# Performance work log

Hardware: AMD Instinct MI355X
Metric: run time of the kernel (lower is better)

## Reference

```python
import jax, jax.numpy as jnp
import numpy as np
from jax import lax

DN = ('NHWC', 'HWIO', 'NHWC')

def _prelu(x, a):
    return jnp.where(x >= 0, x, a * x)

def _conv(x, w, b):
    return lax.conv_general_dilated(x, w, (1, 1), 'VALID', dimension_numbers=DN) + b

def _maxpool(x, k, s, padding):
    # padding: list of (lo, hi) for all 4 dims, or 'VALID'
    return lax.reduce_window(x, -jnp.inf, lax.max, (1, k, k, 1), (1, s, s, 1), padding)

def _onet_forward(x, conv1_w, conv1_b, alpha1, conv2_w, conv2_b, alpha2,
                  conv3_w, conv3_b, alpha3, conv4_w, conv4_b, alpha4,
                  dense5_w, dense5_b, alpha5, w_cls, b_cls, w_box, b_box, w_pts, b_pts):
    # x: [B, 48, 48, 3]
    x = _prelu(_conv(x, conv1_w, conv1_b), alpha1)              # [B,46,46,32]
    # TF 'same' pooling: out=ceil(46/2)=23, total pad 1 -> pad (0,1) bottom/right
    x = _maxpool(x, 3, 2, [(0, 0), (0, 1), (0, 1), (0, 0)])     # [B,23,23,32]
    x = _prelu(_conv(x, conv2_w, conv2_b), alpha2)              # [B,21,21,64]
    x = _maxpool(x, 3, 2, 'VALID')                              # [B,10,10,64]
    x = _prelu(_conv(x, conv3_w, conv3_b), alpha3)              # [B,8,8,64]
    x = _maxpool(x, 2, 2, 'VALID')                              # [B,4,4,64]
    x = _prelu(_conv(x, conv4_w, conv4_b), alpha4)              # [B,3,3,128]
    # Permute((3,2,1)): (H,W,C) -> (C,W,H), then row-major flatten -> 1152
    x = jnp.transpose(x, (0, 3, 2, 1)).reshape(x.shape[0], -1)  # [B,1152]
    x = _prelu(x @ dense5_w + dense5_b, alpha5)                 # [B,256]
    cls = jax.nn.softmax(x @ w_cls + b_cls, axis=-1)            # [B,2]
    roi = x @ w_box + b_box                                     # [B,4]
    pts = x @ w_pts + b_pts                                     # [B,10]
    return cls, roi, pts

def setup_inputs() -> dict:
    key = jax.random.key(0)
    ks = jax.random.split(key, 16)
    N, B = 32, 128
    inputs = jax.random.normal(ks[0], (N, B, 48, 48, 3), dtype=jnp.float32)
    def w(k, shape, fan_in):
        return jax.random.normal(k, shape, dtype=jnp.float32) * (1.0 / np.sqrt(fan_in))
    return {
        'inputs': inputs,
        'conv1_w': w(ks[1], (3, 3, 3, 32), 27),   'conv1_b': jnp.zeros((32,), jnp.float32),  'alpha1': jnp.full((32,), 0.25, jnp.float32),
        'conv2_w': w(ks[2], (3, 3, 32, 64), 288), 'conv2_b': jnp.zeros((64,), jnp.float32),  'alpha2': jnp.full((64,), 0.25, jnp.float32),
        'conv3_w': w(ks[3], (3, 3, 64, 64), 576), 'conv3_b': jnp.zeros((64,), jnp.float32),  'alpha3': jnp.full((64,), 0.25, jnp.float32),
        'conv4_w': w(ks[4], (2, 2, 64, 128), 256),'conv4_b': jnp.zeros((128,), jnp.float32), 'alpha4': jnp.full((128,), 0.25, jnp.float32),
        'dense5_w': w(ks[5], (1152, 256), 1152),  'dense5_b': jnp.zeros((256,), jnp.float32),'alpha5': jnp.full((256,), 0.25, jnp.float32),
        'w_cls': w(ks[6], (256, 2), 256),  'b_cls': jnp.zeros((2,), jnp.float32),
        'w_box': w(ks[7], (256, 4), 256),  'b_box': jnp.zeros((4,), jnp.float32),
        'w_pts': w(ks[8], (256, 10), 256), 'b_pts': jnp.zeros((10,), jnp.float32),
    }

def reference(inputs, conv1_w, conv1_b, alpha1, conv2_w, conv2_b, alpha2,
              conv3_w, conv3_b, alpha3, conv4_w, conv4_b, alpha4,
              dense5_w, dense5_b, alpha5, w_cls, b_cls, w_box, b_box, w_pts, b_pts):
    N, B = inputs.shape[:2]
    x = inputs.reshape(N * B, 48, 48, 3)  # batched instead of tf.map_fn serial loop
    cls, roi, pts = _onet_forward(x, conv1_w, conv1_b, alpha1, conv2_w, conv2_b, alpha2,
                                  conv3_w, conv3_b, alpha3, conv4_w, conv4_b, alpha4,
                                  dense5_w, dense5_b, alpha5, w_cls, b_cls, w_box, b_box, w_pts, b_pts)
    return cls.reshape(N, B, 2), roi.reshape(N, B, 4), pts.reshape(N, B, 10)
```

## Files before the change

### kernel.cpp

```cpp
#include <hip/hip_runtime.h>
#include <hip/hip_bf16.h>

typedef __attribute__((ext_vector_type(8))) short short8;
typedef __attribute__((ext_vector_type(4))) float f32x4;
typedef __attribute__((ext_vector_type(4))) unsigned u32x4;

__device__ __forceinline__ float bf_lo(unsigned v) { return __uint_as_float(v << 16); }
__device__ __forceinline__ float bf_hi(unsigned v) { return __uint_as_float(v & 0xFFFF0000u); }
__device__ __forceinline__ float prelu(float v, float a) { return v >= 0.0f ? v : v * a; }
__device__ __forceinline__ float max3f(float a, float b, float c) { return fmaxf(fmaxf(a, b), c); }

#define P1F   0
#define IN2F  10580
#define CB2F  10580
#define P2F   12596
#define C3F   0
#define P3BF  4096
#define VECF  4672
#define D5F   5824
#define ZZF   6080
#define SMF   18260
#define IN2B  (IN2F * 4)

#define W1T 0
#define W2T 1536
#define W3T 19968
#define W4T 56832
#define W5T 89600
#define WS_ELEMS 384512

__global__ void prep_weights(const float* __restrict__ w1, const float* __restrict__ w2,
                             const float* __restrict__ w3, const float* __restrict__ w4,
                             const float* __restrict__ w5, __hip_bfloat16* __restrict__ ws) {
  int i = blockIdx.x * 256 + threadIdx.x;
  if (i >= WS_ELEMS) return;
  float v = 0.f;
  if (i < W2T) {
    int co = i >> 5, k = i & 31;
    if (k < 27) { int kh = k / 9, r = k % 9, kw = r / 3, ci = r % 3; v = w1[((kh * 3 + kw) * 3 + ci) * 32 + co]; }
  } else if (i < W3T) {
    int j = i - W2T; int khkw = j >> 11, rem = j & 2047, co = rem >> 5, k = rem & 31;
    v = w2[(khkw * 32 + k) * 64 + co];
  } else if (i < W4T) {
    int j = i - W3T; int khkwcg = j >> 11, rem = j & 2047, co = rem >> 5, k = rem & 31;
    v = w3[((khkwcg >> 1) * 64 + (khkwcg & 1) * 32 + k) * 64 + co];
  } else if (i < W5T) {
    int j = i - W4T; int co = j >> 8, k = j & 255; int khkw = k >> 6, ci = k & 63;
    v = w4[(khkw * 64 + ci) * 128 + co];
  } else {
    int j = i - W5T; int jj = j / 1152, k = j - jj * 1152;
    v = w5[k * 256 + jj];
  }
  ws[i] = __float2bfloat16(v);
}

__global__ __launch_bounds__(256, 2)
void onet_kernel(const float* __restrict__ gin,
                 const float* __restrict__ b1, const float* __restrict__ a1,
                 const float* __restrict__ b2, const float* __restrict__ a2,
                 const float* __restrict__ b3, const float* __restrict__ a3,
                 const float* __restrict__ b4, const float* __restrict__ a4,
                 const float* __restrict__ b5, const float* __restrict__ a5,
                 const float* __restrict__ wcls, const float* __restrict__ bcls,
                 const float* __restrict__ wbox, const float* __restrict__ bbox,
                 const float* __restrict__ wpts, const float* __restrict__ bpts,
                 const __hip_bfloat16* __restrict__ ws,
                 float* __restrict__ out, int nimg)
{
  __shared__ __align__(16) float smem[SMF];
  const int t = threadIdx.x;
  const int img = blockIdx.x;
  const int lane = t & 63, wid = t >> 6;
  const int lr = lane & 15, lg = lane >> 4;
  const bool isLg3 = (lg == 3);
  const __hip_bfloat16* w1t = ws + W1T;
  const __hip_bfloat16* w2t = ws + W2T;
  const __hip_bfloat16* w3t = ws + W3T;
  const __hip_bfloat16* w4t = ws + W4T;
  const __hip_bfloat16* w5t = ws + W5T;

  {
    char* sb = (char*)smem + IN2B;
    for (int u = t; u < 48 * 17; u += 256) {
      int row = u / 17, q = u - row * 17;
      char* rp = sb + row * 640;
      if (q < 8)       *(unsigned*)(rp + 288 + 4 * q) = 0u;
      else if (q < 16) *(unsigned*)(rp + 608 + 4 * (q - 8)) = 0u;
      else             *(unsigned short*)(rp + 606) = 0;
    }
    const float* inp = gin + (size_t)img * 6912;
    for (int i = t; i < 6912; i += 256) {
      int h = i / 144, e = i - h * 144;
      unsigned short b = __bfloat16_as_ushort(__float2bfloat16(inp[i]));
      char* rp = sb + h * 640;
      *(unsigned short*)(rp + e * 2) = b;
      if (e) *(unsigned short*)(rp + 320 + (e - 1) * 2) = b;
    }
  }
  __syncthreads();

  {
    short8 bf1c[2];
    float bias1[2], al1[2];
    #pragma unroll
    for (int n = 0; n < 2; ++n) {
      bf1c[n] = *(const short8*)(w1t + (n * 16 + lr) * 32 + 8 * lg);
      bias1[n] = b1[n * 16 + lr];
      al1[n] = a1[n * 16 + lr];
    }
    const unsigned selc = (lg == 1) ? 0x05040100u : 0x03020100u;
    const unsigned m1c = (lg == 3) ? 0x0000FFFFu : ~0u;
    const unsigned mzc = (lg == 3) ? 0u : ~0u;
    int offv[3][5];
    #pragma unroll
    for (int wt = 0; wt < 3; ++wt) {
      int w = 16 * wt + lr;
      int X[5], KH[5];
      if (lg == 0)      { X[0]=3*w;   X[1]=3*w+2; X[2]=3*w+4; X[3]=3*w+6; X[4]=3*w; KH[0]=0;KH[1]=0;KH[2]=0;KH[3]=0;KH[4]=0; }
      else if (lg == 1) { X[0]=3*w+8; X[1]=3*w+1; X[2]=3*w+3; X[3]=3*w+5; X[4]=3*w; KH[0]=0;KH[1]=1;KH[2]=1;KH[3]=1;KH[4]=1; }
      else if (lg == 2) { X[0]=3*w+7; X[1]=3*w;   X[2]=3*w+2; X[3]=3*w+4; X[4]=3*w; KH[0]=1;KH[1]=2;KH[2]=2;KH[3]=2;KH[4]=2; }
      else              { X[0]=3*w+6; X[1]=3*w+8; X[2]=3*w;   X[3]=3*w;   X[4]=3*w; KH[0]=2;KH[1]=2;KH[2]=2;KH[3]=2;KH[4]=2; }
      #pragma unroll
      for (int i = 0; i < 5; ++i)
        offv[wt][i] = KH[i] * 640 + 2 * X[i] + ((X[i] & 1) ? 318 : 0);
    }

    auto compute_row = [&](int h, float (&cur)[3][2][2]) {
      if (h > 45) {
        #pragma unroll
        for (int wt = 0; wt < 3; ++wt)
          #pragma unroll
          for (int n = 0; n < 2; ++n) { cur[wt][n][0] = -1e30f; cur[wt][n][1] = -1e30f; }
        return;
      }
      const char* rowp = (const char*)smem + IN2B + h * 640;
      float v[3][2][4];
      #pragma unroll
      for (int wt = 0; wt < 3; ++wt) {
        unsigned r0 = *(const unsigned*)(rowp + offv[wt][0]);
        unsigned r1 = *(const unsigned*)(rowp + offv[wt][1]);
        unsigned r2 = *(const unsigned*)(rowp + offv[wt][2]);
        unsigned r3 = *(const unsigned*)(rowp + offv[wt][3]);
        unsigned r4 = *(const unsigned*)(rowp + offv[wt][4]);
        u32x4 iv = (u32x4){__builtin_amdgcn_perm(r4, r0, selc), r1 & m1c, r2 & mzc, r3 & mzc};
        short8 af = __builtin_bit_cast(short8, iv);
        #pragma unroll
        for (int n = 0; n < 2; ++n) {
          f32x4 acc = (f32x4){bias1[n], bias1[n], bias1[n], bias1[n]};
          acc = __builtin_amdgcn_mfma_f32_16x16x32_bf16(af, bf1c[n], acc, 0, 0, 0);
          #pragma unroll
          for (int reg = 0; reg < 4; ++reg) v[wt][n][reg] = prelu(acc[reg], al1[n]);
        }
      }
      if (isLg3) {
        #pragma unroll
        for (int n = 0; n < 2; ++n) { v[2][n][2] = -1e30f; v[2][n][3] = -1e30f; }
      }
      #pragma unroll
      for (int n = 0; n < 2; ++n) {
        float hd0 = __shfl_down(v[0][n][0], 16);
        float hd1 = __shfl_down(v[1][n][0], 16);
        float hd2 = __shfl_down(v[2][n][0], 16);
        float hx1 = __shfl(v[1][n][0], lr);
        float hx2 = __shfl(v[2][n][0], lr);
        float h0 = isLg3 ? hx1 : hd0;
        float h1 = isLg3 ? hx2 : hd1;
        cur[0][n][0] = max3f(v[0][n][0], v[0][n][1], v[0][n][2]);
        cur[0][n][1] = max3f(v[0][n][2], v[0][n][3], h0);
        cur[1][n][0] = max3f(v[1][n][0], v[1][n][1], v[1][n][2]);
        cur[1][n][1] = max3f(v[1][n][2], v[1][n][3], h1);
        cur[2][n][0] = max3f(v[2][n][0], v[2][n][1], v[2][n][2]);
        cur[2][n][1] = max3f(v[2][n][2], v[2][n][3], hd2);
      }
    };

    __hip_bfloat16* pool1 = (__hip_bfloat16*)(smem + P1F);
    auto emit = [&](int r, float (&pa)[3][2][2], float (&pb)[3][2][2], float (&pc)[3][2][2]) {
      #pragma unroll
      for (int wt = 0; wt < 3; ++wt)
        #pragma unroll
        for (int n = 0; n < 2; ++n)
          #pragma unroll
          for (int pp = 0; pp < 2; ++pp) {
            float m = max3f(pa[wt][n][pp], pb[wt][n][pp], pc[wt][n][pp]);
            int pw = 8 * wt + 2 * lg + pp;
            if (pw < 23)
              pool1[(r * 23 + pw) * 40 + n * 16 + lr] = __float2bfloat16(m);
          }
    };

    const int pr0 = wid * 6;
    const int pr1 = (pr0 + 5 < 23) ? pr0 + 5 : 22;
    float pa[3][2][2], pb[3][2][2], pc[3][2][2];
    compute_row(2 * pr0, pa);
    compute_row(2 * pr0 + 1, pb);
    for (int r = pr0; r <= pr1; ++r) {
      compute_row(2 * r + 2, pc);
      emit(r, pa, pb, pc);
      if (r < pr1) {
        #pragma unroll
        for (int wt = 0; wt < 3; ++wt)
          #pragma unroll
          for (int n = 0; n < 2; ++n) { pa[wt][n][0] = pc[wt][n][0]; pa[wt][n][1] = pc[wt][n][1]; }
        compute_row(2 * r + 3, pb);
      }
    }
  }
  __syncthreads();

  {
    const __hip_bfloat16* pool1b = (const __hip_bfloat16*)(smem + P1F);
    __hip_bfloat16* cb2 = (__hip_bfloat16*)(smem + CB2F);
    __hip_bfloat16* pool2 = (__hip_bfloat16*)(smem + P2F);
    const int wv = wid;
    short8 bfr[9][4];
    #pragma unroll
    for (int khkw = 0; khkw < 9; ++khkw)
      #pragma unroll
      for (int nt = 0; nt < 4; ++nt)
        bfr[khkw][nt] = *(const short8*)(w2t + ((khkw * 64 + nt * 16 + lr) * 32 + 8 * lg));
    int mA = wv * 16 + lr; if (mA > 62) mA = 62;
    const int krA = mA / 21, owA = mA - krA * 21;
    int mc[4], krc[4], owc[4];
    #pragma unroll
    for (int reg = 0; reg < 4; ++reg) {
      mc[reg] = wv * 16 + lg * 4 + reg;
      krc[reg] = mc[reg] / 21;
      owc[reg] = mc[reg] - krc[reg] * 21;
    }
    float bsn[4], alv[4];
    #pragma unroll
    for (int nt = 0; nt < 4; ++nt) { bsn[nt] = b2[nt * 16 + lr]; alv[nt] = a2[nt * 16 + lr]; }

    for (int r = 0; r < 10; ++r) {
      const int posA = (2 * r + krA) * 23 + owA;
      f32x4 acc[4];
      #pragma unroll
      for (int nt = 0; nt < 4; ++nt) acc[nt] = (f32x4){bsn[nt], bsn[nt], bsn[nt], bsn[nt]};
      #pragma unroll
      for (int kh = 0; kh < 3; ++kh)
        #pragma unroll
        for (int kw = 0; kw < 3; ++kw) {
          short8 af = *(const short8*)(pool1b + (posA + kh * 23 + kw) * 40 + 8 * lg);
          #pragma unroll
          for (int nt = 0; nt < 4; ++nt)
            acc[nt] = __builtin_amdgcn_mfma_f32_16x16x32_bf16(af, bfr[kh * 3 + kw][nt], acc[nt], 0, 0, 0);
        }
      #pragma unroll
      for (int nt = 0; nt < 4; ++nt)
        #pragma unroll
        for (int reg = 0; reg < 4; ++reg)
          if (mc[reg] < 63)
            cb2[(krc[reg] * 21 + owc[reg]) * 64 + nt * 16 + lr] =
                __float2bfloat16(prelu(acc[nt][reg], alv[nt]));
      __syncthreads();
      {
        const int ch = t & 63;
        #pragma unroll
        for (int jj = 0; jj < 3; ++jj) {
          int w = (t >> 6) + 4 * jj;
          if (w < 10) {
            float m = -1e30f;
            #pragma unroll
            for (int kh = 0; kh < 3; ++kh)
              #pragma unroll
              for (int kw = 0; kw < 3; ++kw)
                m = fmaxf(m, __bfloat162float(cb2[(kh * 21 + 2 * w + kw) * 64 + ch]));
            pool2[(r * 10 + w) * 72 + ch] = __float2bfloat16(m);
          }
        }
      }
      __syncthreads();
    }
  }

  {
    const __hip_bfloat16* pool2b = (const __hip_bfloat16*)(smem + P2F);
    float* c3 = smem + C3F;
    const int nt = wid;
    short8 bfr[9][2];
    #pragma unroll
    for (int khkw = 0; khkw < 9; ++khkw)
      #pragma unroll
      for (int cg = 0; cg < 2; ++cg)
        bfr[khkw][cg] = *(const short8*)(w3t + (((khkw * 2 + cg) * 64 + nt * 16 + lr) * 32 + 8 * lg));
    const float bs = b3[nt * 16 + lr], al = a3[nt * 16 + lr];
    #pragma unroll
    for (int mt = 0; mt < 4; ++mt) {
      const int mA = mt * 16 + lr;
      const int ohA = mA >> 3, owA = mA & 7;
      f32x4 acc = (f32x4){bs, bs, bs, bs};
      #pragma unroll
      for (int kh = 0; kh < 3; ++kh)
        #pragma unroll
        for (int kw = 0; kw < 3; ++kw)
          #pragma unroll
          for (int cg = 0; cg < 2; ++cg) {
            short8 af = *(const short8*)(pool2b + ((ohA + kh) * 10 + owA + kw) * 72 + cg * 32 + 8 * lg);
            acc = __builtin_amdgcn_mfma_f32_16x16x32_bf16(af, bfr[kh * 3 + kw][cg], acc, 0, 0, 0);
          }
      #pragma unroll
      for (int reg = 0; reg < 4; ++reg) {
        int m = mt * 16 + lg * 4 + reg;
        c3[m * 64 + nt * 16 + lr] = prelu(acc[reg], al);
      }
    }
  }
  __syncthreads();

  {
    const float* c3 = smem + C3F;
    __hip_bfloat16* pool3b = (__hip_bfloat16*)(smem + P3BF);
    const int c = t & 31;
    const int p = t >> 5;
    #pragma unroll
    for (int j = 0; j < 2; ++j) {
      int pos = p + 8 * j;
      int pi = pos >> 2, pj = pos & 3;
      #pragma unroll
      for (int e = 0; e < 2; ++e) {
        int ch = c + 32 * e;
        float m = fmaxf(
            fmaxf(c3[((2 * pi) * 8 + 2 * pj) * 64 + ch],     c3[((2 * pi) * 8 + 2 * pj + 1) * 64 + ch]),
            fmaxf(c3[((2 * pi + 1) * 8 + 2 * pj) * 64 + ch], c3[((2 * pi + 1) * 8 + 2 * pj + 1) * 64 + ch]));
        pool3b[(pi * 4 + pj) * 72 + ch] = __float2bfloat16(m);
      }
    }
  }
  __syncthreads();

  {
    const __hip_bfloat16* pool3b = (const __hip_bfloat16*)(smem + P3BF);
    float* vec = smem + VECF;
    int pos = lr < 9 ? lr : 8;
    int hh = pos / 3, wwp = pos - hh * 3;
    short8 afr[8];
    #pragma unroll
    for (int s = 0; s < 8; ++s) {
      int khkw = s >> 1, kh = khkw >> 1, kw = khkw & 1;
      int cb = (s & 1) * 32 + 8 * lg;
      afr[s] = *(const short8*)(pool3b + ((hh + kh) * 4 + (wwp + kw)) * 72 + cb);
    }
    #pragma unroll
    for (int q = 0; q < 2; ++q) {
      int co = (wid * 2 + q) * 16 + lr;
      float bb = b4[co];
      f32x4 acc = (f32x4){bb, bb, bb, bb};
      #pragma unroll
      for (int s = 0; s < 8; ++s) {
        short8 bfr = *(const short8*)(w4t + co * 256 + s * 32 + 8 * lg);
        acc = __builtin_amdgcn_mfma_f32_16x16x32_bf16(afr[s], bfr, acc, 0, 0, 0);
      }
      float al = a4[co];
      #pragma unroll
      for (int reg = 0; reg < 4; ++reg) {
        int pp = 4 * lg + reg;
        if (pp < 9) {
          int h9 = pp / 3, w9 = pp - h9 * 3;
          vec[co * 9 + w9 * 3 + h9] = prelu(acc[reg], al);
        }
      }
    }
  }
  __syncthreads();

  {
    const float* vec = smem + VECF;
    float* d5 = smem + D5F;
    const int jj = t;
    const __hip_bfloat16* wrow = w5t + jj * 1152;
    float acc0 = 0.f, acc1 = 0.f, acc2 = 0.f, acc3 = 0.f;
    for (int k = 0; k < 1152; k += 8) {
      uint4 wv = *(const uint4*)(wrow + k);
      float4 x0 = *(const float4*)(vec + k);
      float4 x1 = *(const float4*)(vec + k + 4);
      acc0 = fmaf(x0.x, bf_lo(wv.x), acc0);
      acc1 = fmaf(x0.y, bf_hi(wv.x), acc1);
      acc2 = fmaf(x0.z, bf_lo(wv.y), acc2);
      acc3 = fmaf(x0.w, bf_hi(wv.y), acc3);
      acc0 = fmaf(x1.x, bf_lo(wv.z), acc0);
      acc1 = fmaf(x1.y, bf_hi(wv.z), acc1);
      acc2 = fmaf(x1.z, bf_lo(wv.w), acc2);
      acc3 = fmaf(x1.w, bf_hi(wv.w), acc3);
    }
    float v = (acc0 + acc1) + (acc2 + acc3) + b5[jj];
    d5[jj] = prelu(v, a5[jj]);
  }
  __syncthreads();

  {
    const float* d5 = smem + D5F;
    float* zz = smem + ZZF;
    const int o = t >> 4, s = t & 15;
    float pa = 0.f;
    if (o < 2) {
      for (int k = s; k < 256; k += 16) pa += d5[k] * wcls[k * 2 + o];
    } else if (o < 6) {
      int oc = o - 2;
      for (int k = s; k < 256; k += 16) pa += d5[k] * wbox[k * 4 + oc];
    } else {
      int oc = o - 6;
      for (int k = s; k < 256; k += 16) pa += d5[k] * wpts[k * 10 + oc];
    }
    pa += __shfl_xor(pa, 1);
    pa += __shfl_xor(pa, 2);
    pa += __shfl_xor(pa, 4);
    pa += __shfl_xor(pa, 8);
    if (s == 0) {
      float bias = (o < 2) ? bcls[o] : (o < 6) ? bbox[o - 2] : bpts[o - 6];
      zz[o] = pa + bias;
    }
  }
  __syncthreads();
  if (t < 16) {
    const float* zz = smem + ZZF;
    int o = t;
    if (o < 2) {
      float z0 = zz[0], z1 = zz[1];
      float m = fmaxf(z0, z1);
      float e0 = __expf(z0 - m), e1 = __expf(z1 - m);
      out[(size_t)img * 2 + o] = ((o == 0) ? e0 : e1) / (e0 + e1);
    } else if (o < 6) {
      out[(size_t)nimg * 2 + (size_t)img * 4 + (o - 2)] = zz[o];
    } else {
      out[(size_t)nimg * 6 + (size_t)img * 10 + (o - 6)] = zz[o];
    }
  }
}

extern "C" void kernel_launch(void* const* d_in, const int* in_sizes, int n_in,
                              void* d_out, int out_size, void* d_ws, size_t ws_size,
                              hipStream_t stream) {
  (void)n_in; (void)out_size; (void)ws_size;
  const float* gin  = (const float*)d_in[0];
  const float* w1   = (const float*)d_in[1];
  const float* b1   = (const float*)d_in[2];
  const float* a1   = (const float*)d_in[3];
  const float* w2   = (const float*)d_in[4];
  const float* b2   = (const float*)d_in[5];
  const float* a2   = (const float*)d_in[6];
  const float* w3   = (const float*)d_in[7];
  const float* b3   = (const float*)d_in[8];
  const float* a3   = (const float*)d_in[9];
  const float* w4   = (const float*)d_in[10];
  const float* b4   = (const float*)d_in[11];
  const float* a4   = (const float*)d_in[12];
  const float* w5   = (const float*)d_in[13];
  const float* b5   = (const float*)d_in[14];
  const float* a5   = (const float*)d_in[15];
  const float* wcls = (const float*)d_in[16];
  const float* bcls = (const float*)d_in[17];
  const float* wbox = (const float*)d_in[18];
  const float* bbox = (const float*)d_in[19];
  const float* wpts = (const float*)d_in[20];
  const float* bpts = (const float*)d_in[21];
  float* out = (float*)d_out;
  __hip_bfloat16* wst = (__hip_bfloat16*)d_ws;
  const int nimg = in_sizes[0] / 6912;

  prep_weights<<<(WS_ELEMS + 255) / 256, 256, 0, stream>>>(w1, w2, w3, w4, w5, wst);
  onet_kernel<<<nimg, 256, 0, stream>>>(gin, b1, a1, b2, a2, b3, a3,
                                        b4, a4, b5, a5,
                                        wcls, bcls, wbox, bbox, wpts, bpts,
                                        wst, out, nimg);
}
```

Baseline: 816.1 us.

## Split dense layers into batched MFMA kernel and shrink conv LDS footprint

The dense5 layer and heads move out of the per-image conv kernel into a separate kernel. It processes 16 images per block with bf16 MFMA, so the 1152x256 weight matrix is reused across images instead of streamed per image with scalar FMAs. The conv kernel loads the input in three row phases so it fits a smaller LDS buffer. It fuses pool3 into the conv3 epilogue via shuffles and raises launch bounds to 3 blocks per CU. The trade-off is a global intermediate buffer (a fixed 4096-image device array), an extra launch, extra syncs, and bf16 rounding of the dense input.

Result: faster. 750.4 us (-8.0%).

```diff
diff --git a/kernel.cpp b/kernel.cpp
--- a/kernel.cpp
+++ b/kernel.cpp
@@ -10,17 +10,8 @@
 __device__ __forceinline__ float prelu(float v, float a) { return v >= 0.0f ? v : v * a; }
 __device__ __forceinline__ float max3f(float a, float b, float c) { return fmaxf(fmaxf(a, b), c); }
 
-#define P1F   0
-#define IN2F  10580
-#define CB2F  10580
-#define P2F   12596
-#define C3F   0
-#define P3BF  4096
-#define VECF  4672
-#define D5F   5824
-#define ZZF   6080
-#define SMF   18260
-#define IN2B  (IN2F * 4)
+#define XB   42320
+#define SMB  53584
 
 #define W1T 0
 #define W2T 1536
@@ -28,6 +19,8 @@
 #define W4T 56832
 #define W5T 89600
 #define WS_ELEMS 384512
+
+__device__ __hip_bfloat16 vec_g[4096ull * 1152];
 
 __global__ void prep_weights(const float* __restrict__ w1, const float* __restrict__ w2,
                              const float* __restrict__ w3, const float* __restrict__ w4,
@@ -54,20 +47,15 @@
   ws[i] = __float2bfloat16(v);
 }
 
-__global__ __launch_bounds__(256, 2)
+__global__ __launch_bounds__(256, 3)
 void onet_kernel(const float* __restrict__ gin,
                  const float* __restrict__ b1, const float* __restrict__ a1,
                  const float* __restrict__ b2, const float* __restrict__ a2,
                  const float* __restrict__ b3, const float* __restrict__ a3,
                  const float* __restrict__ b4, const float* __restrict__ a4,
-                 const float* __restrict__ b5, const float* __restrict__ a5,
-                 const float* __restrict__ wcls, const float* __restrict__ bcls,
-                 const float* __restrict__ wbox, const float* __restrict__ bbox,
-                 const float* __restrict__ wpts, const float* __restrict__ bpts,
-                 const __hip_bfloat16* __restrict__ ws,
-                 float* __restrict__ out, int nimg)
+                 const __hip_bfloat16* __restrict__ ws, int nimg)
 {
-  __shared__ __align__(16) float smem[SMF];
+  __shared__ __align__(16) char smemc[SMB];
   const int t = threadIdx.x;
   const int img = blockIdx.x;
   const int lane = t & 63, wid = t >> 6;
@@ -77,29 +65,10 @@
   const __hip_bfloat16* w2t = ws + W2T;
   const __hip_bfloat16* w3t = ws + W3T;
   const __hip_bfloat16* w4t = ws + W4T;
-  const __hip_bfloat16* w5t = ws + W5T;
-
-  {
-    char* sb = (char*)smem + IN2B;
-    for (int u = t; u < 48 * 17; u += 256) {
-      int row = u / 17, q = u - row * 17;
-      char* rp = sb + row * 640;
-      if (q < 8)       *(unsigned*)(rp + 288 + 4 * q) = 0u;
-      else if (q < 16) *(unsigned*)(rp + 608 + 4 * (q - 8)) = 0u;
-      else             *(unsigned short*)(rp + 606) = 0;
-    }
-    const float* inp = gin + (size_t)img * 6912;
-    for (int i = t; i < 6912; i += 256) {
-      int h = i / 144, e = i - h * 144;
-      unsigned short b = __bfloat16_as_ushort(__float2bfloat16(inp[i]));
-      char* rp = sb + h * 640;
-      *(unsigned short*)(rp + e * 2) = b;
-      if (e) *(unsigned short*)(rp + 320 + (e - 1) * 2) = b;
-    }
-  }
-  __syncthreads();
-
-  {
+
+  {
+    __hip_bfloat16* pool1 = (__hip_bfloat16*)smemc;
+    char* in2 = smemc + XB;
     short8 bf1c[2];
     float bias1[2], al1[2];
     #pragma unroll
@@ -122,10 +91,10 @@
       else              { X[0]=3*w+6; X[1]=3*w+8; X[2]=3*w;   X[3]=3*w;   X[4]=3*w; KH[0]=2;KH[1]=2;KH[2]=2;KH[3]=2;KH[4]=2; }
       #pragma unroll
       for (int i = 0; i < 5; ++i)
-        offv[wt][i] = KH[i] * 640 + 2 * X[i] + ((X[i] & 1) ? 318 : 0);
-    }
-
-    auto compute_row = [&](int h, float (&cur)[3][2][2]) {
+        offv[wt][i] = KH[i] * 592 + 2 * X[i] + ((X[i] & 1) ? 294 : 0);
+    }
+
+    auto compute_row = [&](int h, int base, float (&cur)[3][2][2]) {
       if (h > 45) {
         #pragma unroll
         for (int wt = 0; wt < 3; ++wt)
@@ -133,7 +102,7 @@
           for (int n = 0; n < 2; ++n) { cur[wt][n][0] = -1e30f; cur[wt][n][1] = -1e30f; }
         return;
       }
-      const char* rowp = (const char*)smem + IN2B + h * 640;
+      const char* rowp = in2 + (h - base) * 592;
       float v[3][2][4];
       #pragma unroll
       for (int wt = 0; wt < 3; ++wt) {
@@ -174,7 +143,6 @@
       }
     };
 
-    __hip_bfloat16* pool1 = (__hip_bfloat16*)(smem + P1F);
     auto emit = [&](int r, float (&pa)[3][2][2], float (&pb)[3][2][2], float (&pc)[3][2][2]) {
       #pragma unroll
       for (int wt = 0; wt < 3; ++wt)
@@ -189,29 +157,58 @@
           }
     };
 
-    const int pr0 = wid * 6;
-    const int pr1 = (pr0 + 5 < 23) ? pr0 + 5 : 22;
-    float pa[3][2][2], pb[3][2][2], pc[3][2][2];
-    compute_row(2 * pr0, pa);
-    compute_row(2 * pr0 + 1, pb);
-    for (int r = pr0; r <= pr1; ++r) {
-      compute_row(2 * r + 2, pc);
-      emit(r, pa, pb, pc);
-      if (r < pr1) {
-        #pragma unroll
-        for (int wt = 0; wt < 3; ++wt)
-          #pragma unroll
-          for (int n = 0; n < 2; ++n) { pa[wt][n][0] = pc[wt][n][0]; pa[wt][n][1] = pc[wt][n][1]; }
-        compute_row(2 * r + 3, pb);
+    for (int u = t; u < 95; u += 256) {
+      int row = u / 5, q = u - row * 5;
+      char* rp = in2 + row * 592;
+      if (q < 2)      *(unsigned*)(rp + 288 + 4 * q) = 0u;
+      else if (q < 4) *(unsigned*)(rp + 584 + 4 * (q - 2)) = 0u;
+      else            *(unsigned short*)(rp + 582) = 0;
+    }
+
+    const int base_[3]  = {0, 14, 30};
+    const int nrows_[3] = {17, 19, 18};
+    const int lo_[3]    = {0, 7, 15};
+    const int hi_[3]    = {6, 14, 22};
+    for (int ph = 0; ph < 3; ++ph) {
+      if (ph) __syncthreads();
+      const int base = base_[ph];
+      {
+        const float* inp = gin + (size_t)img * 6912 + base * 144;
+        const int ne = nrows_[ph] * 144;
+        for (int i = t; i < ne; i += 256) {
+          int rl = i / 144, e = i - rl * 144;
+          unsigned short b = __bfloat16_as_ushort(__float2bfloat16(inp[i]));
+          char* rp = in2 + rl * 592;
+          *(unsigned short*)(rp + 2 * e) = b;
+          if (e) *(unsigned short*)(rp + 2 * e + 294) = b;
+        }
+      }
+      __syncthreads();
+      int r0 = lo_[ph] + 2 * wid;
+      if (r0 <= hi_[ph]) {
+        int r1 = (r0 + 1 <= hi_[ph]) ? r0 + 1 : r0;
+        float pa[3][2][2], pb[3][2][2], pc[3][2][2];
+        compute_row(2 * r0,     base, pa);
+        compute_row(2 * r0 + 1, base, pb);
+        compute_row(2 * r0 + 2, base, pc);
+        emit(r0, pa, pb, pc);
+        if (r1 > r0) {
+          #pragma unroll
+          for (int wt = 0; wt < 3; ++wt)
+            #pragma unroll
+            for (int n = 0; n < 2; ++n) { pa[wt][n][0] = pc[wt][n][0]; pa[wt][n][1] = pc[wt][n][1]; }
+          compute_row(2 * r0 + 3, base, pb);
+          compute_row(2 * r0 + 4, base, pc);
+          emit(r1, pa, pb, pc);
+        }
       }
     }
   }
   __syncthreads();
 
   {
-    const __hip_bfloat16* pool1b = (const __hip_bfloat16*)(smem + P1F);
-    __hip_bfloat16* cb2 = (__hip_bfloat16*)(smem + CB2F);
-    __hip_bfloat16* pool2 = (__hip_bfloat16*)(smem + P2F);
+    const __hip_bfloat16* pool1b = (const __hip_bfloat16*)smemc;
+    __hip_bfloat16* cb2 = (__hip_bfloat16*)(smemc + XB);
     const int wv = wid;
     short8 bfr[9][4];
     #pragma unroll
@@ -266,7 +263,7 @@
               #pragma unroll
               for (int kw = 0; kw < 3; ++kw)
                 m = fmaxf(m, __bfloat162float(cb2[(kh * 21 + 2 * w + kw) * 64 + ch]));
-            pool2[(r * 10 + w) * 72 + ch] = __float2bfloat16(m);
+            *(__hip_bfloat16*)(smemc + r * 3680 + w * 144 + ch * 2) = __float2bfloat16(m);
           }
         }
       }
@@ -275,8 +272,7 @@
   }
 
   {
-    const __hip_bfloat16* pool2b = (const __hip_bfloat16*)(smem + P2F);
-    float* c3 = smem + C3F;
+    __hip_bfloat16* pool3b = (__hip_bfloat16*)(smemc + XB);
     const int nt = wid;
     short8 bfr[9][2];
     #pragma unroll
@@ -296,42 +292,25 @@
         for (int kw = 0; kw < 3; ++kw)
           #pragma unroll
           for (int cg = 0; cg < 2; ++cg) {
-            short8 af = *(const short8*)(pool2b + ((ohA + kh) * 10 + owA + kw) * 72 + cg * 32 + 8 * lg);
+            short8 af = *(const short8*)(smemc + (ohA + kh) * 3680 + (owA + kw) * 144 + cg * 64 + lg * 16);
             acc = __builtin_amdgcn_mfma_f32_16x16x32_bf16(af, bfr[kh * 3 + kw][cg], acc, 0, 0, 0);
           }
-      #pragma unroll
-      for (int reg = 0; reg < 4; ++reg) {
-        int m = mt * 16 + lg * 4 + reg;
-        c3[m * 64 + nt * 16 + lr] = prelu(acc[reg], al);
+      float v0 = prelu(acc[0], al), v1 = prelu(acc[1], al);
+      float v2 = prelu(acc[2], al), v3 = prelu(acc[3], al);
+      float h01 = fmaxf(v0, v1), h23 = fmaxf(v2, v3);
+      float p01 = fmaxf(h01, __shfl_xor(h01, 32));
+      float p23 = fmaxf(h23, __shfl_xor(h23, 32));
+      if (lg < 2) {
+        pool3b[(mt * 4 + 2 * lg + 0) * 72 + nt * 16 + lr] = __float2bfloat16(p01);
+        pool3b[(mt * 4 + 2 * lg + 1) * 72 + nt * 16 + lr] = __float2bfloat16(p23);
       }
     }
   }
   __syncthreads();
 
   {
-    const float* c3 = smem + C3F;
-    __hip_bfloat16* pool3b = (__hip_bfloat16*)(smem + P3BF);
-    const int c = t & 31;
-    const int p = t >> 5;
-    #pragma unroll
-    for (int j = 0; j < 2; ++j) {
-      int pos = p + 8 * j;
-      int pi = pos >> 2, pj = pos & 3;
-      #pragma unroll
-      for (int e = 0; e < 2; ++e) {
-        int ch = c + 32 * e;
-        float m = fmaxf(
-            fmaxf(c3[((2 * pi) * 8 + 2 * pj) * 64 + ch],     c3[((2 * pi) * 8 + 2 * pj + 1) * 64 + ch]),
-            fmaxf(c3[((2 * pi + 1) * 8 + 2 * pj) * 64 + ch], c3[((2 * pi + 1) * 8 + 2 * pj + 1) * 64 + ch]));
-        pool3b[(pi * 4 + pj) * 72 + ch] = __float2bfloat16(m);
-      }
-    }
-  }
-  __syncthreads();
-
-  {
-    const __hip_bfloat16* pool3b = (const __hip_bfloat16*)(smem + P3BF);
-    float* vec = smem + VECF;
+    const __hip_bfloat16* pool3b = (const __hip_bfloat16*)(smemc + XB);
+    __hip_bfloat16* vg = vec_g + (size_t)img * 1152;
     int pos = lr < 9 ? lr : 8;
     int hh = pos / 3, wwp = pos - hh * 3;
     short8 afr[8];
@@ -357,73 +336,97 @@
         int pp = 4 * lg + reg;
         if (pp < 9) {
           int h9 = pp / 3, w9 = pp - h9 * 3;
-          vec[co * 9 + w9 * 3 + h9] = prelu(acc[reg], al);
-        }
-      }
+          vg[co * 9 + w9 * 3 + h9] = __float2bfloat16(prelu(acc[reg], al));
+        }
+      }
+    }
+  }
+}
+
+__global__ __launch_bounds__(256, 2)
+void dense_kernel(const __hip_bfloat16* __restrict__ ws,
+                  const float* __restrict__ b5, const float* __restrict__ a5,
+                  const float* __restrict__ wcls, const float* __restrict__ bcls,
+                  const float* __restrict__ wbox, const float* __restrict__ bbox,
+                  const float* __restrict__ wpts, const float* __restrict__ bpts,
+                  float* __restrict__ out, int nimg)
+{
+  __shared__ __align__(16) char asm_[16 * 1160 * 2];
+  __shared__ float d5s[16][257];
+  __shared__ float zz[16][17];
+  const int t = threadIdx.x;
+  const int lane = t & 63, wid = t >> 6;
+  const int lr = lane & 15, lg = lane >> 4;
+  const int blk = blockIdx.x;
+  const __hip_bfloat16* w5t = ws + W5T;
+
+  {
+    const __hip_bfloat16* src = vec_g + (size_t)blk * 16 * 1152;
+    for (int i = t; i < 16 * 144; i += 256) {
+      int im = i / 144, kq = i - im * 144;
+      *(uint4*)(asm_ + (im * 1160 + kq * 8) * 2) = *(const uint4*)(src + im * 1152 + kq * 8);
     }
   }
   __syncthreads();
 
-  {
-    const float* vec = smem + VECF;
-    float* d5 = smem + D5F;
-    const int jj = t;
-    const __hip_bfloat16* wrow = w5t + jj * 1152;
-    float acc0 = 0.f, acc1 = 0.f, acc2 = 0.f, acc3 = 0.f;
-    for (int k = 0; k < 1152; k += 8) {
-      uint4 wv = *(const uint4*)(wrow + k);
-      float4 x0 = *(const float4*)(vec + k);
-      float4 x1 = *(const float4*)(vec + k + 4);
-      acc0 = fmaf(x0.x, bf_lo(wv.x), acc0);
-      acc1 = fmaf(x0.y, bf_hi(wv.x), acc1);
-      acc2 = fmaf(x0.z, bf_lo(wv.y), acc2);
-      acc3 = fmaf(x0.w, bf_hi(wv.y), acc3);
-      acc0 = fmaf(x1.x, bf_lo(wv.z), acc0);
-      acc1 = fmaf(x1.y, bf_hi(wv.z), acc1);
-      acc2 = fmaf(x1.z, bf_lo(wv.w), acc2);
-      acc3 = fmaf(x1.w, bf_hi(wv.w), acc3);
-    }
-    float v = (acc0 + acc1) + (acc2 + acc3) + b5[jj];
-    d5[jj] = prelu(v, a5[jj]);
-  }
+  f32x4 acc[4];
+  float av[4];
+  int jjv[4];
+  #pragma unroll
+  for (int q = 0; q < 4; ++q) {
+    jjv[q] = (wid * 4 + q) * 16 + lr;
+    float bv = b5[jjv[q]];
+    av[q] = a5[jjv[q]];
+    acc[q] = (f32x4){bv, bv, bv, bv};
+  }
+  for (int ks = 0; ks < 36; ++ks) {
+    short8 af = *(const short8*)(asm_ + lr * 2320 + ks * 64 + lg * 16);
+    #pragma unroll
+    for (int q = 0; q < 4; ++q) {
+      short8 bf = *(const short8*)(w5t + jjv[q] * 1152 + ks * 32 + 8 * lg);
+      acc[q] = __builtin_amdgcn_mfma_f32_16x16x32_bf16(af, bf, acc[q], 0, 0, 0);
+    }
+  }
+  #pragma unroll
+  for (int q = 0; q < 4; ++q)
+    #pragma unroll
+    for (int reg = 0; reg < 4; ++reg) {
+      int im = 4 * lg + reg;
+      d5s[im][jjv[q]] = prelu(acc[q][reg], av[q]);
+    }
   __syncthreads();
 
   {
-    const float* d5 = smem + D5F;
-    float* zz = smem + ZZF;
-    const int o = t >> 4, s = t & 15;
-    float pa = 0.f;
+    const int im = t >> 4, o = t & 15;
+    float z;
     if (o < 2) {
-      for (int k = s; k < 256; k += 16) pa += d5[k] * wcls[k * 2 + o];
+      z = bcls[o];
+      #pragma unroll 4
+      for (int k = 0; k < 256; ++k) z += d5s[im][k] * wcls[k * 2 + o];
     } else if (o < 6) {
-      int oc = o - 2;
-      for (int k = s; k < 256; k += 16) pa += d5[k] * wbox[k * 4 + oc];
+      z = bbox[o - 2];
+      #pragma unroll 4
+      for (int k = 0; k < 256; ++k) z += d5s[im][k] * wbox[k * 4 + (o - 2)];
     } else {
-      int oc = o - 6;
-      for (int k = s; k < 256; k += 16) pa += d5[k] * wpts[k * 10 + oc];
-    }
-    pa += __shfl_xor(pa, 1);
-    pa += __shfl_xor(pa, 2);
-    pa += __shfl_xor(pa, 4);
-    pa += __shfl_xor(pa, 8);
-    if (s == 0) {
-      float bias = (o < 2) ? bcls[o] : (o < 6) ? bbox[o - 2] : bpts[o - 6];
-      zz[o] = pa + bias;
-    }
+      z = bpts[o - 6];
+      #pragma unroll 4
+      for (int k = 0; k < 256; ++k) z += d5s[im][k] * wpts[k * 10 + (o - 6)];
+    }
+    zz[im][o] = z;
   }
   __syncthreads();
-  if (t < 16) {
-    const float* zz = smem + ZZF;
-    int o = t;
+  {
+    const int im = t >> 4, o = t & 15;
+    size_t ig = (size_t)blk * 16 + im;
     if (o < 2) {
-      float z0 = zz[0], z1 = zz[1];
+      float z0 = zz[im][0], z1 = zz[im][1];
       float m = fmaxf(z0, z1);
       float e0 = __expf(z0 - m), e1 = __expf(z1 - m);
-      out[(size_t)img * 2 + o] = ((o == 0) ? e0 : e1) / (e0 + e1);
+      out[ig * 2 + o] = ((o == 0) ? e0 : e1) / (e0 + e1);
     } else if (o < 6) {
-      out[(size_t)nimg * 2 + (size_t)img * 4 + (o - 2)] = zz[o];
+      out[(size_t)nimg * 2 + ig * 4 + (o - 2)] = zz[im][o];
     } else {
-      out[(size_t)nimg * 6 + (size_t)img * 10 + (o - 6)] = zz[o];
+      out[(size_t)nimg * 6 + ig * 10 + (o - 6)] = zz[im][o];
     }
   }
 }
@@ -459,8 +462,7 @@
   const int nimg = in_sizes[0] / 6912;
 
   prep_weights<<<(WS_ELEMS + 255) / 256, 256, 0, stream>>>(w1, w2, w3, w4, w5, wst);
-  onet_kernel<<<nimg, 256, 0, stream>>>(gin, b1, a1, b2, a2, b3, a3,
-                                        b4, a4, b5, a5,
-                                        wcls, bcls, wbox, bbox, wpts, bpts,
-                                        wst, out, nimg);
+  onet_kernel<<<nimg, 256, 0, stream>>>(gin, b1, a1, b2, a2, b3, a3, b4, a4, wst, nimg);
+  dense_kernel<<<nimg / 16, 256, 0, stream>>>(wst, b5, a5, wcls, bcls, wbox, bbox,
+                                              wpts, bpts, out, nimg);
 }
```
